# Kernel tuning notes

Measured on AMD Instinct MI355X. Metric: run time of the kernel, lower is better.

Reference implementation:

```python
import jax, jax.numpy as jnp
import numpy as np
import math

DIM = 2048
N_HEADS = 16
HEAD_DIM = 128
BATCH = 2
T = 2048
EPS = 1e-5


def setup_inputs() -> dict:
    key = jax.random.key(0)
    ks = jax.random.split(key, 16)
    s = lambda fan_in: 1.0 / math.sqrt(fan_in)
    d = {}
    d['x'] = jax.random.normal(ks[0], (BATCH, T, DIM), dtype=jnp.float32)
    d['start_pos'] = 0
    # attention projections (weights stored [in, out])
    d['wq'] = jax.random.uniform(ks[1], (DIM, N_HEADS * HEAD_DIM), minval=-s(DIM), maxval=s(DIM))
    d['bq'] = jnp.zeros((N_HEADS * HEAD_DIM,), jnp.float32)
    d['wk'] = jax.random.uniform(ks[2], (DIM, HEAD_DIM), minval=-s(DIM), maxval=s(DIM))
    d['bk'] = jnp.zeros((HEAD_DIM,), jnp.float32)
    d['wv'] = jax.random.uniform(ks[3], (DIM, HEAD_DIM), minval=-s(DIM), maxval=s(DIM))
    d['bv'] = jnp.zeros((HEAD_DIM,), jnp.float32)
    d['wo'] = jax.random.uniform(ks[4], (N_HEADS * HEAD_DIM, DIM), minval=-s(N_HEADS * HEAD_DIM), maxval=s(N_HEADS * HEAD_DIM))
    d['bo'] = jnp.zeros((DIM,), jnp.float32)
    # layernorms
    d['ln1_g'] = jnp.ones((DIM,), jnp.float32)
    d['ln1_b'] = jnp.zeros((DIM,), jnp.float32)
    d['ln2_g'] = jnp.ones((DIM,), jnp.float32)
    d['ln2_b'] = jnp.zeros((DIM,), jnp.float32)
    # MLP (dim -> 4*dim -> dim), dropout p=0 is a no-op
    d['w1'] = jax.random.uniform(ks[5], (DIM, 4 * DIM), minval=-s(DIM), maxval=s(DIM))
    d['b1'] = jnp.zeros((4 * DIM,), jnp.float32)
    d['w2'] = jax.random.uniform(ks[6], (4 * DIM, DIM), minval=-s(4 * DIM), maxval=s(4 * DIM))
    d['b2'] = jnp.zeros((DIM,), jnp.float32)
    return d


def _layernorm(h, g, b):
    mu = jnp.mean(h, axis=-1, keepdims=True)
    var = jnp.mean(jnp.square(h - mu), axis=-1, keepdims=True)
    return (h - mu) * jax.lax.rsqrt(var + EPS) * g + b


def reference(x, start_pos, wq, bq, wk, bk, wv, bv, wo, bo, ln1_g, ln1_b, ln2_g, ln2_b, w1, b1, w2, b2):
    B, Tq, D = x.shape
    hd = wk.shape[1]
    H = wq.shape[1] // hd
    # --- MQA attention on pre-LN input (prefill: no kv cache) ---
    h = _layernorm(x, ln1_g, ln1_b)
    q = (h @ wq + bq).reshape(B, Tq, H, hd)          # [B,T,H,hd]
    k = h @ wk + bk                                   # [B,T,hd] single shared head
    v = h @ wv + bv                                   # [B,T,hd]
    scores = jnp.einsum('bthc,bsc->bhts', q, k) / math.sqrt(hd)
    causal = jnp.where(jnp.tril(jnp.ones((Tq, Tq), dtype=bool)), 0.0, -jnp.inf).astype(scores.dtype)
    attn = jax.nn.softmax(scores + causal, axis=-1)   # [B,H,T,T]
    ctx = jnp.einsum('bhts,bsc->bthc', attn, v).reshape(B, Tq, H * hd)
    out = ctx @ wo + bo
    x = x + out
    # --- GELU MLP (exact erf gelu, torch default) ---
    h2 = _layernorm(x, ln2_g, ln2_b)
    x = x + jax.nn.gelu(h2 @ w1 + b1, approximate=False) @ w2 + b2
    k_cat = k[:, None]                                # [B,1,T,hd]
    v_cat = v[:, None]
    return (x, k_cat, v_cat)
```

## Files before the change

### kernel.cpp

```cpp
#include <hip/hip_runtime.h>
#include <stdint.h>

#define DIMSZ 2048
#define HD 128
#define NH 16
#define BATCH 2
#define SEQ 2048
#define MROWS (BATCH*SEQ)
#define FFDIM (4*DIMSZ)
#define NQKV (DIMSZ + 2*HD)

typedef float f32x4 __attribute__((ext_vector_type(4)));
typedef __bf16 bf16x8 __attribute__((ext_vector_type(8)));
typedef __bf16 bf16_t;

__device__ __forceinline__ void async16(const void* g, void* l) {
  __builtin_amdgcn_global_load_lds(
      (const __attribute__((address_space(1))) void*)(uintptr_t)g,
      (__attribute__((address_space(3))) void*)(uint32_t)(uintptr_t)l,
      16, 0, 0);
}

__device__ __forceinline__ float gelu_f(float x) {
  return 0.5f * x * (1.0f + erff(x * 0.70710678118654752f));
}

__device__ __forceinline__ void hard_barrier() {
  asm volatile("" ::: "memory");
  __builtin_amdgcn_s_barrier();
  asm volatile("" ::: "memory");
}

__global__ __launch_bounds__(256)
void k_transpose_f32_bf16(const float* __restrict__ src, bf16_t* __restrict__ dst,
                          int R, int C) {
  __shared__ float tile[32][33];
  int c0 = blockIdx.x * 32, r0 = blockIdx.y * 32;
  int tx = threadIdx.x & 31, ty = threadIdx.x >> 5;
#pragma unroll
  for (int i = 0; i < 32; i += 8)
    tile[ty + i][tx] = src[(size_t)(r0 + ty + i) * C + (c0 + tx)];
  __syncthreads();
#pragma unroll
  for (int i = 0; i < 32; i += 8)
    dst[(size_t)(c0 + ty + i) * R + (r0 + tx)] = (bf16_t)tile[tx][ty + i];
}

__global__ __launch_bounds__(256)
void k_transpose_v(const bf16_t* __restrict__ v, bf16_t* __restrict__ vt) {
  __shared__ bf16_t tile[32][33];
  int b = blockIdx.z;
  int t0 = blockIdx.x * 32, d0 = blockIdx.y * 32;
  int tx = threadIdx.x & 31, ty = threadIdx.x >> 5;
#pragma unroll
  for (int i = 0; i < 32; i += 8)
    tile[ty + i][tx] = v[((size_t)(b * SEQ + t0 + ty + i)) * HD + d0 + tx];
  __syncthreads();
#pragma unroll
  for (int i = 0; i < 32; i += 8)
    vt[((size_t)(b * HD + d0 + ty + i)) * SEQ + t0 + tx] = tile[tx][ty + i];
}

__global__ __launch_bounds__(256)
void k_layernorm(const float* __restrict__ x, const float* __restrict__ g,
                 const float* __restrict__ bb, bf16_t* __restrict__ out) {
  int row = blockIdx.x;
  const float* xr = x + (size_t)row * DIMSZ;
  int t = threadIdx.x;
  float vals[8];
  float s = 0.f, s2 = 0.f;
#pragma unroll
  for (int i = 0; i < 8; ++i) {
    float v = xr[t + i * 256];
    vals[i] = v; s += v; s2 += v * v;
  }
#pragma unroll
  for (int o = 1; o < 64; o <<= 1) { s += __shfl_xor(s, o); s2 += __shfl_xor(s2, o); }
  __shared__ float red[8];
  if ((t & 63) == 0) { red[t >> 6] = s; red[4 + (t >> 6)] = s2; }
  __syncthreads();
  s = red[0] + red[1] + red[2] + red[3];
  s2 = red[4] + red[5] + red[6] + red[7];
  float mu = s * (1.0f / DIMSZ);
  float rstd = rsqrtf(s2 * (1.0f / DIMSZ) - mu * mu + 1e-5f);
  bf16_t* orow = out + (size_t)row * DIMSZ;
#pragma unroll
  for (int i = 0; i < 8; ++i) {
    int c = t + i * 256;
    orow[c] = (bf16_t)((vals[i] - mu) * rstd * g[c] + bb[c]);
  }
}

template <int FN>
__device__ __forceinline__ void gemm8_loop(
    const bf16_t* __restrict__ A, const bf16_t* __restrict__ BT,
    int ld, int Kloop, int bm, int bn, f32x4 (&acc)[8][FN], bf16_t* sh) {
  constexpr int BH = FN >> 1;
  constexpr int BN = FN * 64;
  const int tid = threadIdx.x;
  const int lane = tid & 63, lr = lane & 15, lg = lane >> 4;
  const int wave = tid >> 6, wm = wave >> 2, wn = wave & 3;
  bf16_t* const Ab0 = sh;
  bf16_t* const Bb0 = sh + 32768;
  const bf16_t* const Ag = A + (size_t)bm * 256 * ld;
  const bf16_t* const Bg = BT + (size_t)bn * BN * ld;

  auto stage = [&](const bf16_t* gbase, bf16_t* lbase, int h, int t) {
#pragma unroll
    for (int j = 0; j < 2; ++j) {
      int flat = (tid + j * 512) * 8;
      int r = flat >> 6, kp = flat & 63;
      int ks = kp ^ ((r & 7) << 3);
      async16(gbase + (size_t)(h * 128 + r) * ld + t * 64 + ks, lbase + flat);
    }
  };
  auto stA = [&](int c, int h, int t) { stage(Ag, Ab0 + (c * 2 + h) * 8192, h, t); };
  auto stB = [&](int c, int h, int t) { stage(Bg, Bb0 + (c * BH + h) * 8192, h, t); };

  const int xsw = (lr & 7) << 3;
  bf16x8 a_[8], b_[FN][2];
  auto lda = [&](int c, int kk) {
    const bf16_t* base = Ab0 + (c * 2 + wm) * 8192;
#pragma unroll
    for (int mf = 0; mf < 8; ++mf)
      a_[mf] = *(const bf16x8*)(base + (mf * 16 + lr) * 64 + ((kk + lg * 8) ^ xsw));
  };
  auto ldb = [&](int c) {
#pragma unroll
    for (int nf = 0; nf < FN; ++nf) {
      int row = wn * (FN * 16) + nf * 16 + lr;
      const bf16_t* base =
          Bb0 + (c * BH + (BH == 2 ? (row >> 7) : 0)) * 8192 + (row & 127) * 64;
#pragma unroll
      for (int kx = 0; kx < 2; ++kx)
        b_[nf][kx] = *(const bf16x8*)(base + ((kx * 32 + lg * 8) ^ xsw));
    }
  };

#define LGKM0 asm volatile("s_waitcnt lgkmcnt(0)" ::: "memory");
#define VMC_STEADY                                                   \
  if (BH == 2) { asm volatile("s_waitcnt vmcnt(6)" ::: "memory"); }  \
  else         { asm volatile("s_waitcnt vmcnt(4)" ::: "memory"); }
#define MFMA_HALF(M0, KX)                                            \
  __builtin_amdgcn_s_setprio(1);                                     \
  _Pragma("unroll")                                                  \
  for (int mf = 0; mf < 4; ++mf)                                     \
    _Pragma("unroll")                                                \
    for (int nf = 0; nf < FN; ++nf)                                  \
      acc[(M0) + mf][nf] = __builtin_amdgcn_mfma_f32_16x16x32_bf16(  \
          a_[(M0) + mf], b_[nf][KX], acc[(M0) + mf][nf], 0, 0, 0);   \
  __builtin_amdgcn_s_setprio(0);

  const int nit = Kloop >> 7;

  stA(0, 0, 0); stA(0, 1, 0);
  stB(0, 0, 0); if (BH == 2) stB(0, 1, 0);
  stB(1, 0, 1); if (BH == 2) stB(1, 1, 1);
  stA(1, 0, 1);
  VMC_STEADY;
  hard_barrier();

  for (int i = 0; i < nit; ++i) {
    const int t1 = 2 * i + 1, t2 = 2 * i + 2, t3 = 2 * i + 3;
    const bool g2 = (i < nit - 1);
    lda(0, 0); ldb(0);
    stA(1, 1, t1);
    hard_barrier(); LGKM0;
    MFMA_HALF(0, 0)
    hard_barrier();
    if (g2) stB(0, 0, t2);
    hard_barrier();
    MFMA_HALF(4, 0)
    hard_barrier();
    lda(0, 32);
    if (g2 && BH == 2) stB(0, 1, t2);
    hard_barrier(); LGKM0;
    MFMA_HALF(0, 1)
    hard_barrier();
    if (g2) stA(0, 0, t2);
    if (i == nit - 1) { asm volatile("s_waitcnt vmcnt(0)" ::: "memory"); }
    else { VMC_STEADY; }
    hard_barrier();
    MFMA_HALF(4, 1)
    hard_barrier();
    lda(1, 0); ldb(1);
    if (g2) stA(0, 1, t2);
    hard_barrier(); LGKM0;
    MFMA_HALF(0, 0)
    hard_barrier();
    if (g2) stB(1, 0, t3);
    hard_barrier();
    MFMA_HALF(4, 0)
    hard_barrier();
    lda(1, 32);
    if (g2 && BH == 2) stB(1, 1, t3);
    hard_barrier(); LGKM0;
    MFMA_HALF(0, 1)
    hard_barrier();
    if (g2) {
      stA(1, 0, t3);
      VMC_STEADY;
    }
    hard_barrier();
    MFMA_HALF(4, 1)
    hard_barrier();
  }
#undef LGKM0
#undef VMC_STEADY
#undef MFMA_HALF
}

__global__ __launch_bounds__(512, 1)
void k_oproj(const bf16_t* __restrict__ A, const bf16_t* __restrict__ BT,
             const float* __restrict__ bias, const float* __restrict__ res,
             float* __restrict__ outF) {
  extern __shared__ __align__(16) bf16_t sh8[];
  const int nt = DIMSZ / 128;
  int bm = blockIdx.x / nt, bn = blockIdx.x % nt;
  f32x4 acc[8][2] = {};
  gemm8_loop<2>(A, BT, DIMSZ, DIMSZ, bm, bn, acc, sh8);
  int tid = threadIdx.x, wave = tid >> 6, lane = tid & 63, lr = lane & 15, lg = lane >> 4;
  int wm = wave >> 2, wn = wave & 3;
  int row0 = bm * 256 + wm * 128 + lg * 4;
  int col0 = bn * 128 + wn * 32 + lr;
#pragma unroll
  for (int nf = 0; nf < 2; ++nf) {
    int c = col0 + nf * 16;
    float bi = bias[c];
#pragma unroll
    for (int mf = 0; mf < 8; ++mf)
#pragma unroll
      for (int j = 0; j < 4; ++j) {
        int r = row0 + mf * 16 + j;
        size_t idx = (size_t)r * DIMSZ + c;
        outF[idx] = acc[mf][nf][j] + bi + res[idx];
      }
  }
}

__global__ __launch_bounds__(512, 1)
void k_ffn1(const bf16_t* __restrict__ A, const bf16_t* __restrict__ BT,
            const float* __restrict__ bias, bf16_t* __restrict__ outB) {
  extern __shared__ __align__(16) bf16_t sh8[];
  const int nt = FFDIM / 256;
  int bm = blockIdx.x / nt, bn = blockIdx.x % nt;
  f32x4 acc[8][4] = {};
  gemm8_loop<4>(A, BT, DIMSZ, DIMSZ, bm, bn, acc, sh8);
  int tid = threadIdx.x, wave = tid >> 6, lane = tid & 63, lr = lane & 15, lg = lane >> 4;
  int wm = wave >> 2, wn = wave & 3;
  int row0 = bm * 256 + wm * 128 + lg * 4;
  int col0 = bn * 256 + wn * 64 + lr;
#pragma unroll
  for (int nf = 0; nf < 4; ++nf) {
    int c = col0 + nf * 16;
    float bi = bias[c];
#pragma unroll
    for (int mf = 0; mf < 8; ++mf)
#pragma unroll
      for (int j = 0; j < 4; ++j) {
        int r = row0 + mf * 16 + j;
        outB[(size_t)r * FFDIM + c] = (bf16_t)gelu_f(acc[mf][nf][j] + bi);
      }
  }
}

__global__ __launch_bounds__(512, 1)
void k_ffn2(const bf16_t* __restrict__ A, const bf16_t* __restrict__ BT,
            const float* __restrict__ bias, float* __restrict__ outF) {
  extern __shared__ __align__(16) bf16_t sh8[];
  int bid = blockIdx.x;
  int kh = bid >> 7;
  int tile = bid & 127;
  int bm = tile >> 3, bn = tile & 7;
  f32x4 acc[8][4] = {};
  gemm8_loop<4>(A + kh * (FFDIM / 2), BT + kh * (FFDIM / 2), FFDIM, FFDIM / 2,
                bm, bn, acc, sh8);
  int tid = threadIdx.x, wave = tid >> 6, lane = tid & 63, lr = lane & 15, lg = lane >> 4;
  int wm = wave >> 2, wn = wave & 3;
  int row0 = bm * 256 + wm * 128 + lg * 4;
  int col0 = bn * 256 + wn * 64 + lr;
#pragma unroll
  for (int nf = 0; nf < 4; ++nf) {
    int c = col0 + nf * 16;
    float bi = kh ? 0.f : bias[c];
#pragma unroll
    for (int mf = 0; mf < 8; ++mf)
#pragma unroll
      for (int j = 0; j < 4; ++j) {
        int r = row0 + mf * 16 + j;
        __hip_atomic_fetch_add(&outF[(size_t)r * DIMSZ + c], acc[mf][nf][j] + bi,
                               __ATOMIC_RELAXED, __HIP_MEMORY_SCOPE_AGENT);
      }
  }
}

__global__ __launch_bounds__(512, 1)
void k_qkv(const bf16_t* __restrict__ A, const bf16_t* __restrict__ BT,
           const float* __restrict__ bq, const float* __restrict__ bk,
           const float* __restrict__ bv,
           bf16_t* __restrict__ qb, float* __restrict__ outk,
           float* __restrict__ outv, bf16_t* __restrict__ kbf,
           bf16_t* __restrict__ vbf) {
  extern __shared__ __align__(16) bf16_t sh8[];
  const int nt = NQKV / 256;
  int bm = blockIdx.x / nt, bn = blockIdx.x % nt;
  f32x4 acc[8][4] = {};
  gemm8_loop<4>(A, BT, DIMSZ, DIMSZ, bm, bn, acc, sh8);
  int tid = threadIdx.x, wave = tid >> 6, lane = tid & 63, lr = lane & 15, lg = lane >> 4;
  int wm = wave >> 2, wn = wave & 3;
  int row0 = bm * 256 + wm * 128 + lg * 4;
  int col0 = bn * 256 + wn * 64 + lr;
#pragma unroll
  for (int nf = 0; nf < 4; ++nf) {
    int c = col0 + nf * 16;
    float bi = (c < 2048) ? bq[c] : (c < 2176 ? bk[c - 2048] : bv[c - 2176]);
#pragma unroll
    for (int mf = 0; mf < 8; ++mf) {
#pragma unroll
      for (int j = 0; j < 4; ++j) {
        int r = row0 + mf * 16 + j;
        float v = acc[mf][nf][j] + bi;
        if (c < 2048) {
          qb[(size_t)r * DIMSZ + c] = (bf16_t)v;
        } else if (c < 2176) {
          int cc = c - 2048;
          outk[(size_t)r * HD + cc] = v;
          kbf[(size_t)r * HD + cc] = (bf16_t)v;
        } else {
          int cc = c - 2176;
          outv[(size_t)r * HD + cc] = v;
          vbf[(size_t)r * HD + cc] = (bf16_t)v;
        }
      }
    }
  }
}

__global__ __launch_bounds__(256, 2)
void k_attn(const bf16_t* __restrict__ q, const bf16_t* __restrict__ k,
            const bf16_t* __restrict__ vt, bf16_t* __restrict__ ctx) {
  __shared__ __align__(16) bf16_t Ks[2][64 * 128];
  __shared__ __align__(16) bf16_t Vs[2][128 * 64];
  __shared__ bf16_t Pw[4][16][72];
  int pp = blockIdx.x, h = blockIdx.y, b = blockIdx.z;
  int tid = threadIdx.x, wave = tid >> 6, lane = tid & 63, lr = lane & 15, lg = lane >> 4;
  const bf16_t* kb = k + (size_t)b * SEQ * HD;
  const bf16_t* vb = vt + (size_t)b * HD * SEQ;

#define STAGE_TILE(buf, s0_)                                                      \
  {                                                                               \
    _Pragma("unroll")                                                             \
    for (int i = 0; i < 4; ++i) {                                                 \
      int flat = (i * 256 + tid) * 8;                                             \
      int kr = flat >> 7, kc = flat & 127;                                        \
      int ksrc = (((kc >> 3) ^ (kr & 7)) << 3) | (kc & 7);                        \
      async16(kb + (size_t)((s0_) + kr) * HD + ksrc, (void*)(Ks[buf] + flat));    \
      int vr = flat >> 6, vc = flat & 63;                                         \
      int vsrc = (((vc >> 3) ^ (vr & 7)) << 3) | (vc & 7);                        \
      async16(vb + (size_t)vr * SEQ + (s0_) + vsrc, (void*)(Vs[buf] + flat));     \
    }                                                                             \
  }

  for (int half = 0; half < 2; ++half) {
    int qt = half ? (31 - pp) : pp;
    int q0 = qt * 64;
    int qw = q0 + wave * 16;
    const bf16_t* qbase = q + ((size_t)(b * SEQ + qw + lr)) * DIMSZ + h * HD;
    bf16x8 qf[4];
#pragma unroll
    for (int kk = 0; kk < 4; ++kk) qf[kk] = *(const bf16x8*)(qbase + kk * 32 + lg * 8);
    f32x4 o[8] = {};
    float m_[4], l_[4];
#pragma unroll
    for (int j = 0; j < 4; ++j) { m_[j] = -3.0e38f; l_[j] = 0.f; }
    int qglob0 = qw + lg * 4;
    int ntiles = qt + 1;

    STAGE_TILE(0, 0)
    __syncthreads();
    for (int t = 0; t < ntiles; ++t) {
      int cur = t & 1;
      if (t + 1 < ntiles) STAGE_TILE(cur ^ 1, (t + 1) * 64)
      int s0 = t * 64;
      const bf16_t* Kc = Ks[cur];
      const bf16_t* Vc = Vs[cur];
      f32x4 sf[4] = {};
#pragma unroll
      for (int nf = 0; nf < 4; ++nf) {
        int R = nf * 16 + lr;
#pragma unroll
        for (int kk = 0; kk < 4; ++kk)
          sf[nf] = __builtin_amdgcn_mfma_f32_16x16x32_bf16(
              qf[kk],
              *(const bf16x8*)(Kc + R * 128 + (((kk * 4 + lg) ^ (R & 7)) << 3)),
              sf[nf], 0, 0, 0);
      }
#pragma unroll
      for (int nf = 0; nf < 4; ++nf) {
        int col = s0 + nf * 16 + lr;
#pragma unroll
        for (int j = 0; j < 4; ++j) {
          float v = sf[nf][j] * 0.088388347648318447f;
          sf[nf][j] = (col <= qglob0 + j) ? v : -3.0e38f;
        }
      }
      float mx[4];
#pragma unroll
      for (int j = 0; j < 4; ++j)
        mx[j] = fmaxf(fmaxf(sf[0][j], sf[1][j]), fmaxf(sf[2][j], sf[3][j]));
#pragma unroll
      for (int o_ = 1; o_ < 16; o_ <<= 1)
#pragma unroll
        for (int j = 0; j < 4; ++j) mx[j] = fmaxf(mx[j], __shfl_xor(mx[j], o_));
      float fsc[4], mn[4];
#pragma unroll
      for (int j = 0; j < 4; ++j) {
        mn[j] = fmaxf(m_[j], mx[j]);
        fsc[j] = __expf(m_[j] - mn[j]);
        m_[j] = mn[j];
      }
      float ps[4] = {0.f, 0.f, 0.f, 0.f};
#pragma unroll
      for (int nf = 0; nf < 4; ++nf)
#pragma unroll
        for (int j = 0; j < 4; ++j) {
          float pv = __expf(sf[nf][j] - mn[j]);
          ps[j] += pv;
          Pw[wave][lg * 4 + j][nf * 16 + lr] = (bf16_t)pv;
        }
#pragma unroll
      for (int o_ = 1; o_ < 16; o_ <<= 1)
#pragma unroll
        for (int j = 0; j < 4; ++j) ps[j] += __shfl_xor(ps[j], o_);
#pragma unroll
      for (int j = 0; j < 4; ++j) l_[j] = l_[j] * fsc[j] + ps[j];
#pragma unroll
      for (int df = 0; df < 8; ++df)
#pragma unroll
        for (int j = 0; j < 4; ++j) o[df][j] *= fsc[j];
      asm volatile("" ::: "memory");
      bf16x8 pa[2];
#pragma unroll
      for (int kk = 0; kk < 2; ++kk)
        pa[kk] = *(const bf16x8*)(&Pw[wave][lr][kk * 32 + lg * 8]);
#pragma unroll
      for (int df = 0; df < 8; ++df) {
        int R = df * 16 + lr;
#pragma unroll
        for (int kk = 0; kk < 2; ++kk)
          o[df] = __builtin_amdgcn_mfma_f32_16x16x32_bf16(
              pa[kk],
              *(const bf16x8*)(Vc + R * 64 + (((kk * 4 + lg) ^ (R & 7)) << 3)),
              o[df], 0, 0, 0);
      }
      __syncthreads();
    }
    bf16_t* cb = ctx + ((size_t)(b * SEQ + qw)) * DIMSZ + h * HD;
#pragma unroll
    for (int df = 0; df < 8; ++df)
#pragma unroll
      for (int j = 0; j < 4; ++j)
        cb[(size_t)(lg * 4 + j) * DIMSZ + df * 16 + lr] = (bf16_t)(o[df][j] / l_[j]);
  }
#undef STAGE_TILE
}

extern "C" void kernel_launch(void* const* d_in, const int* in_sizes, int n_in,
                              void* d_out, int out_size, void* d_ws, size_t ws_size,
                              hipStream_t stream) {
  const float* x   = (const float*)d_in[0];
  const float* wq  = (const float*)d_in[2];
  const float* bq  = (const float*)d_in[3];
  const float* wk  = (const float*)d_in[4];
  const float* bk  = (const float*)d_in[5];
  const float* wv  = (const float*)d_in[6];
  const float* bv  = (const float*)d_in[7];
  const float* wo  = (const float*)d_in[8];
  const float* bo  = (const float*)d_in[9];
  const float* g1  = (const float*)d_in[10];
  const float* be1 = (const float*)d_in[11];
  const float* g2  = (const float*)d_in[12];
  const float* be2 = (const float*)d_in[13];
  const float* w1  = (const float*)d_in[14];
  const float* bb1 = (const float*)d_in[15];
  const float* w2  = (const float*)d_in[16];
  const float* bb2 = (const float*)d_in[17];

  float* outx = (float*)d_out;
  float* outk = outx + (size_t)MROWS * DIMSZ;
  float* outv = outk + (size_t)MROWS * HD;

  char* p = (char*)d_ws;
  auto alloc = [&](size_t bytes) -> char* {
    char* r = p;
    p += (bytes + 255) & ~(size_t)255;
    return r;
  };
  bf16_t* wqkvT = (bf16_t*)alloc((size_t)NQKV * DIMSZ * 2);
  bf16_t* woT = (bf16_t*)alloc((size_t)DIMSZ * DIMSZ * 2);
  bf16_t* w1T = (bf16_t*)alloc((size_t)FFDIM * DIMSZ * 2);
  bf16_t* w2T = (bf16_t*)alloc((size_t)DIMSZ * FFDIM * 2);
  bf16_t* hb  = (bf16_t*)alloc((size_t)MROWS * DIMSZ * 2);
  bf16_t* qb  = (bf16_t*)alloc((size_t)MROWS * DIMSZ * 2);
  bf16_t* kbf = (bf16_t*)alloc((size_t)MROWS * HD * 2);
  bf16_t* vbf = (bf16_t*)alloc((size_t)MROWS * HD * 2);
  bf16_t* vtb = (bf16_t*)alloc((size_t)BATCH * HD * SEQ * 2);
  bf16_t* f1b = (bf16_t*)alloc((size_t)MROWS * FFDIM * 2);
  (void)ws_size; (void)in_sizes; (void)n_in; (void)out_size;

  dim3 blk(256);
  const int LDS4 = 131072;
  const int LDS2 = 98304;
  k_transpose_f32_bf16<<<dim3(DIMSZ / 32, DIMSZ / 32), blk, 0, stream>>>(wq, wqkvT, DIMSZ, DIMSZ);
  k_transpose_f32_bf16<<<dim3(HD / 32, DIMSZ / 32), blk, 0, stream>>>(wk, wqkvT + (size_t)2048 * DIMSZ, DIMSZ, HD);
  k_transpose_f32_bf16<<<dim3(HD / 32, DIMSZ / 32), blk, 0, stream>>>(wv, wqkvT + (size_t)2176 * DIMSZ, DIMSZ, HD);
  k_transpose_f32_bf16<<<dim3(DIMSZ / 32, DIMSZ / 32), blk, 0, stream>>>(wo, woT, DIMSZ, DIMSZ);
  k_transpose_f32_bf16<<<dim3(FFDIM / 32, DIMSZ / 32), blk, 0, stream>>>(w1, w1T, DIMSZ, FFDIM);
  k_transpose_f32_bf16<<<dim3(DIMSZ / 32, FFDIM / 32), blk, 0, stream>>>(w2, w2T, FFDIM, DIMSZ);
  k_layernorm<<<MROWS, blk, 0, stream>>>(x, g1, be1, hb);
  k_qkv<<<(MROWS / 256) * (NQKV / 256), 512, LDS4, stream>>>(
      hb, wqkvT, bq, bk, bv, qb, outk, outv, kbf, vbf);
  k_transpose_v<<<dim3(SEQ / 32, HD / 32, BATCH), blk, 0, stream>>>(vbf, vtb);
  k_attn<<<dim3(SEQ / 64 / 2, NH, BATCH), blk, 0, stream>>>(qb, kbf, vtb, hb);
  k_oproj<<<(MROWS / 256) * (DIMSZ / 128), 512, LDS2, stream>>>(hb, woT, bo, x, outx);
  k_layernorm<<<MROWS, blk, 0, stream>>>(outx, g2, be2, qb);
  k_ffn1<<<(MROWS / 256) * (FFDIM / 256), 512, LDS4, stream>>>(qb, w1T, bb1, f1b);
  k_ffn2<<<256, 512, LDS4, stream>>>(f1b, w2T, bb2, outx);
}
```

Baseline: 585.1 us.

## Stage GEMM epilogues through LDS, add XCD block swizzle, widen weight transpose

GEMM epilogues (qkv, oproj, ffn1) now write accumulators into shared memory and then issue coalesced 16-byte global stores, replacing scattered scalar stores. Block indices are remapped so consecutive tiles land on the same XCD, which should improve L2 reuse. The weight transpose moves to 64x64 tiles with packed bf16x2 stores. oproj now requests 128KB of LDS, so its staging buffer fits; the cost is an extra barrier and LDS round trip in each epilogue.

```diff
diff --git a/kernel.cpp b/kernel.cpp
--- a/kernel.cpp
+++ b/kernel.cpp
@@ -12,6 +12,7 @@
 
 typedef float f32x4 __attribute__((ext_vector_type(4)));
 typedef __bf16 bf16x8 __attribute__((ext_vector_type(8)));
+typedef __bf16 bf16x2 __attribute__((ext_vector_type(2)));
 typedef __bf16 bf16_t;
 
 __device__ __forceinline__ void async16(const void* g, void* l) {
@@ -31,19 +32,27 @@
   asm volatile("" ::: "memory");
 }
 
+__device__ __forceinline__ int xcd_swz(int bid, int nwg) {
+  return (bid & 7) * (nwg >> 3) + (bid >> 3);
+}
+
 __global__ __launch_bounds__(256)
-void k_transpose_f32_bf16(const float* __restrict__ src, bf16_t* __restrict__ dst,
-                          int R, int C) {
-  __shared__ float tile[32][33];
-  int c0 = blockIdx.x * 32, r0 = blockIdx.y * 32;
-  int tx = threadIdx.x & 31, ty = threadIdx.x >> 5;
-#pragma unroll
-  for (int i = 0; i < 32; i += 8)
-    tile[ty + i][tx] = src[(size_t)(r0 + ty + i) * C + (c0 + tx)];
+void k_tr64(const float* __restrict__ src, bf16_t* __restrict__ dst,
+            int R, int C) {
+  __shared__ float tile[64][65];
+  int c0 = blockIdx.x * 64, r0 = blockIdx.y * 64;
+  int lc = threadIdx.x & 63, lrow = threadIdx.x >> 6;
+#pragma unroll
+  for (int i = 0; i < 64; i += 4)
+    tile[lrow + i][lc] = src[(size_t)(r0 + lrow + i) * C + c0 + lc];
   __syncthreads();
-#pragma unroll
-  for (int i = 0; i < 32; i += 8)
-    dst[(size_t)(c0 + ty + i) * R + (r0 + tx)] = (bf16_t)tile[tx][ty + i];
+  int rp = threadIdx.x & 31, wc = threadIdx.x >> 5;
+#pragma unroll
+  for (int i = 0; i < 64; i += 8) {
+    int c = wc + i;
+    bf16x2 pk = {(bf16_t)tile[2 * rp][c], (bf16_t)tile[2 * rp + 1][c]};
+    *(bf16x2*)(dst + (size_t)(c0 + c) * R + r0 + 2 * rp) = pk;
+  }
 }
 
 __global__ __launch_bounds__(256)
@@ -216,25 +225,36 @@
              float* __restrict__ outF) {
   extern __shared__ __align__(16) bf16_t sh8[];
   const int nt = DIMSZ / 128;
-  int bm = blockIdx.x / nt, bn = blockIdx.x % nt;
+  const int nwg = (MROWS / 256) * nt;
+  int swz = xcd_swz(blockIdx.x, nwg);
+  int bm = swz / nt, bn = swz % nt;
   f32x4 acc[8][2] = {};
   gemm8_loop<2>(A, BT, DIMSZ, DIMSZ, bm, bn, acc, sh8);
   int tid = threadIdx.x, wave = tid >> 6, lane = tid & 63, lr = lane & 15, lg = lane >> 4;
   int wm = wave >> 2, wn = wave & 3;
-  int row0 = bm * 256 + wm * 128 + lg * 4;
-  int col0 = bn * 128 + wn * 32 + lr;
+  float* shF = (float*)sh8;
+  int rl0 = wm * 128 + lg * 4;
+  int cl0 = wn * 32 + lr;
 #pragma unroll
   for (int nf = 0; nf < 2; ++nf) {
-    int c = col0 + nf * 16;
-    float bi = bias[c];
+    int cl = cl0 + nf * 16;
+    float bi = bias[bn * 128 + cl];
 #pragma unroll
     for (int mf = 0; mf < 8; ++mf)
 #pragma unroll
-      for (int j = 0; j < 4; ++j) {
-        int r = row0 + mf * 16 + j;
-        size_t idx = (size_t)r * DIMSZ + c;
-        outF[idx] = acc[mf][nf][j] + bi + res[idx];
-      }
+      for (int j = 0; j < 4; ++j)
+        shF[(rl0 + mf * 16 + j) * 128 + cl] = acc[mf][nf][j] + bi;
+  }
+  hard_barrier();
+  const float* rbase = res + (size_t)(bm * 256) * DIMSZ + bn * 128;
+  float* gbase = outF + (size_t)(bm * 256) * DIMSZ + bn * 128;
+#pragma unroll
+  for (int s = 0; s < 16; ++s) {
+    int flat = s * 512 + tid;
+    int row = flat >> 5, cu = flat & 31;
+    f32x4 v = *(const f32x4*)(shF + row * 128 + cu * 4);
+    f32x4 r4 = *(const f32x4*)(rbase + (size_t)row * DIMSZ + cu * 4);
+    *(f32x4*)(gbase + (size_t)row * DIMSZ + cu * 4) = v + r4;
   }
 }
 
@@ -243,24 +263,33 @@
             const float* __restrict__ bias, bf16_t* __restrict__ outB) {
   extern __shared__ __align__(16) bf16_t sh8[];
   const int nt = FFDIM / 256;
-  int bm = blockIdx.x / nt, bn = blockIdx.x % nt;
+  const int nwg = (MROWS / 256) * nt;
+  int swz = xcd_swz(blockIdx.x, nwg);
+  int bm = swz / nt, bn = swz % nt;
   f32x4 acc[8][4] = {};
   gemm8_loop<4>(A, BT, DIMSZ, DIMSZ, bm, bn, acc, sh8);
   int tid = threadIdx.x, wave = tid >> 6, lane = tid & 63, lr = lane & 15, lg = lane >> 4;
   int wm = wave >> 2, wn = wave & 3;
-  int row0 = bm * 256 + wm * 128 + lg * 4;
-  int col0 = bn * 256 + wn * 64 + lr;
+  int rl0 = wm * 128 + lg * 4;
+  int cl0 = wn * 64 + lr;
 #pragma unroll
   for (int nf = 0; nf < 4; ++nf) {
-    int c = col0 + nf * 16;
-    float bi = bias[c];
+    int cl = cl0 + nf * 16;
+    float bi = bias[bn * 256 + cl];
 #pragma unroll
     for (int mf = 0; mf < 8; ++mf)
 #pragma unroll
-      for (int j = 0; j < 4; ++j) {
-        int r = row0 + mf * 16 + j;
-        outB[(size_t)r * FFDIM + c] = (bf16_t)gelu_f(acc[mf][nf][j] + bi);
-      }
+      for (int j = 0; j < 4; ++j)
+        sh8[(rl0 + mf * 16 + j) * 256 + cl] = (bf16_t)gelu_f(acc[mf][nf][j] + bi);
+  }
+  hard_barrier();
+  bf16_t* gbase = outB + (size_t)(bm * 256) * FFDIM + bn * 256;
+#pragma unroll
+  for (int s = 0; s < 16; ++s) {
+    int flat = s * 512 + tid;
+    int row = flat >> 5, cu = flat & 31;
+    f32x4 v = *(const f32x4*)(sh8 + row * 256 + cu * 8);
+    *(f32x4*)(gbase + (size_t)row * FFDIM + cu * 8) = v;
   }
 }
 
@@ -268,9 +297,9 @@
 void k_ffn2(const bf16_t* __restrict__ A, const bf16_t* __restrict__ BT,
             const float* __restrict__ bias, float* __restrict__ outF) {
   extern __shared__ __align__(16) bf16_t sh8[];
-  int bid = blockIdx.x;
-  int kh = bid >> 7;
-  int tile = bid & 127;
+  int swz = xcd_swz(blockIdx.x, 256);
+  int kh = swz >> 7;
+  int tile = swz & 127;
   int bm = tile >> 3, bn = tile & 7;
   f32x4 acc[8][4] = {};
   gemm8_loop<4>(A + kh * (FFDIM / 2), BT + kh * (FFDIM / 2), FFDIM, FFDIM / 2,
@@ -303,35 +332,46 @@
            bf16_t* __restrict__ vbf) {
   extern __shared__ __align__(16) bf16_t sh8[];
   const int nt = NQKV / 256;
-  int bm = blockIdx.x / nt, bn = blockIdx.x % nt;
+  const int nwg = (MROWS / 256) * nt;
+  int swz = xcd_swz(blockIdx.x, nwg);
+  int bm = swz / nt, bn = swz % nt;
   f32x4 acc[8][4] = {};
   gemm8_loop<4>(A, BT, DIMSZ, DIMSZ, bm, bn, acc, sh8);
   int tid = threadIdx.x, wave = tid >> 6, lane = tid & 63, lr = lane & 15, lg = lane >> 4;
   int wm = wave >> 2, wn = wave & 3;
-  int row0 = bm * 256 + wm * 128 + lg * 4;
-  int col0 = bn * 256 + wn * 64 + lr;
+  int rl0 = wm * 128 + lg * 4;
+  int cl0 = wn * 64 + lr;
 #pragma unroll
   for (int nf = 0; nf < 4; ++nf) {
-    int c = col0 + nf * 16;
-    float bi = (c < 2048) ? bq[c] : (c < 2176 ? bk[c - 2048] : bv[c - 2176]);
-#pragma unroll
-    for (int mf = 0; mf < 8; ++mf) {
+    int cl = cl0 + nf * 16;
+    int cg = bn * 256 + cl;
+    float bi = (cg < 2048) ? bq[cg] : (cg < 2176 ? bk[cg - 2048] : bv[cg - 2176]);
+#pragma unroll
+    for (int mf = 0; mf < 8; ++mf)
 #pragma unroll
       for (int j = 0; j < 4; ++j) {
-        int r = row0 + mf * 16 + j;
         float v = acc[mf][nf][j] + bi;
-        if (c < 2048) {
-          qb[(size_t)r * DIMSZ + c] = (bf16_t)v;
-        } else if (c < 2176) {
-          int cc = c - 2048;
-          outk[(size_t)r * HD + cc] = v;
-          kbf[(size_t)r * HD + cc] = (bf16_t)v;
-        } else {
-          int cc = c - 2176;
-          outv[(size_t)r * HD + cc] = v;
-          vbf[(size_t)r * HD + cc] = (bf16_t)v;
+        sh8[(rl0 + mf * 16 + j) * 256 + cl] = (bf16_t)v;
+        if (cg >= 2048) {
+          int r = bm * 256 + rl0 + mf * 16 + j;
+          if (cg < 2176) outk[(size_t)r * HD + (cg - 2048)] = v;
+          else           outv[(size_t)r * HD + (cg - 2176)] = v;
         }
       }
+  }
+  hard_barrier();
+#pragma unroll
+  for (int s = 0; s < 16; ++s) {
+    int flat = s * 512 + tid;
+    int row = flat >> 5, cu = flat & 31;
+    f32x4 v = *(const f32x4*)(sh8 + row * 256 + cu * 8);
+    int r = bm * 256 + row;
+    if (bn < 8) {
+      *(f32x4*)(qb + (size_t)r * DIMSZ + bn * 256 + cu * 8) = v;
+    } else {
+      int ce = cu * 8;
+      if (ce < 128) *(f32x4*)(kbf + (size_t)r * HD + ce) = v;
+      else          *(f32x4*)(vbf + (size_t)r * HD + (ce - 128)) = v;
     }
   }
 }
@@ -509,21 +549,20 @@
   (void)ws_size; (void)in_sizes; (void)n_in; (void)out_size;
 
   dim3 blk(256);
-  const int LDS4 = 131072;
-  const int LDS2 = 98304;
-  k_transpose_f32_bf16<<<dim3(DIMSZ / 32, DIMSZ / 32), blk, 0, stream>>>(wq, wqkvT, DIMSZ, DIMSZ);
-  k_transpose_f32_bf16<<<dim3(HD / 32, DIMSZ / 32), blk, 0, stream>>>(wk, wqkvT + (size_t)2048 * DIMSZ, DIMSZ, HD);
-  k_transpose_f32_bf16<<<dim3(HD / 32, DIMSZ / 32), blk, 0, stream>>>(wv, wqkvT + (size_t)2176 * DIMSZ, DIMSZ, HD);
-  k_transpose_f32_bf16<<<dim3(DIMSZ / 32, DIMSZ / 32), blk, 0, stream>>>(wo, woT, DIMSZ, DIMSZ);
-  k_transpose_f32_bf16<<<dim3(FFDIM / 32, DIMSZ / 32), blk, 0, stream>>>(w1, w1T, DIMSZ, FFDIM);
-  k_transpose_f32_bf16<<<dim3(DIMSZ / 32, FFDIM / 32), blk, 0, stream>>>(w2, w2T, FFDIM, DIMSZ);
+  const int LDSG = 131072;
+  k_tr64<<<dim3(DIMSZ / 64, DIMSZ / 64), blk, 0, stream>>>(wq, wqkvT, DIMSZ, DIMSZ);
+  k_tr64<<<dim3(HD / 64, DIMSZ / 64), blk, 0, stream>>>(wk, wqkvT + (size_t)2048 * DIMSZ, DIMSZ, HD);
+  k_tr64<<<dim3(HD / 64, DIMSZ / 64), blk, 0, stream>>>(wv, wqkvT + (size_t)2176 * DIMSZ, DIMSZ, HD);
+  k_tr64<<<dim3(DIMSZ / 64, DIMSZ / 64), blk, 0, stream>>>(wo, woT, DIMSZ, DIMSZ);
+  k_tr64<<<dim3(FFDIM / 64, DIMSZ / 64), blk, 0, stream>>>(w1, w1T, DIMSZ, FFDIM);
+  k_tr64<<<dim3(DIMSZ / 64, FFDIM / 64), blk, 0, stream>>>(w2, w2T, FFDIM, DIMSZ);
   k_layernorm<<<MROWS, blk, 0, stream>>>(x, g1, be1, hb);
-  k_qkv<<<(MROWS / 256) * (NQKV / 256), 512, LDS4, stream>>>(
+  k_qkv<<<(MROWS / 256) * (NQKV / 256), 512, LDSG, stream>>>(
       hb, wqkvT, bq, bk, bv, qb, outk, outv, kbf, vbf);
   k_transpose_v<<<dim3(SEQ / 32, HD / 32, BATCH), blk, 0, stream>>>(vbf, vtb);
   k_attn<<<dim3(SEQ / 64 / 2, NH, BATCH), blk, 0, stream>>>(qb, kbf, vtb, hb);
-  k_oproj<<<(MROWS / 256) * (DIMSZ / 128), 512, LDS2, stream>>>(hb, woT, bo, x, outx);
+  k_oproj<<<(MROWS / 256) * (DIMSZ / 128), 512, LDSG, stream>>>(hb, woT, bo, x, outx);
   k_layernorm<<<MROWS, blk, 0, stream>>>(outx, g2, be2, qb);
-  k_ffn1<<<(MROWS / 256) * (FFDIM / 256), 512, LDS4, stream>>>(qb, w1T, bb1, f1b);
-  k_ffn2<<<256, 512, LDS4, stream>>>(f1b, w2T, bb2, outx);
-}
+  k_ffn1<<<(MROWS / 256) * (FFDIM / 256), 512, LDSG, stream>>>(qb, w1T, bb1, f1b);
+  k_ffn2<<<256, 512, LDSG, stream>>>(f1b, w2T, bb2, outx);
+}
```

Result: faster. 560.9 us (-4.1%).
